# Optimization experiments

Measured on AMD Instinct MI355X. Metric: run time of the kernel, lower is better.

The kernel has to match this reference:

```python
import jax, jax.numpy as jnp
import numpy as np

LAMBD = 1.0
N_CLASSES = 1000


def setup_inputs() -> dict:
    key = jax.random.key(0)
    k1, k2, k3 = jax.random.split(key, 3)
    B, D, C = 32768, 128, N_CLASSES
    embeddings = jax.random.normal(k1, (B, D), dtype=jnp.float32)
    targets = jax.random.randint(k2, (B,), 0, C, dtype=jnp.int64)
    centers = jax.random.normal(k3, (C, D), dtype=jnp.float32)
    return {"embeddings": embeddings, "targets": targets, "centers": centers}


def reference(embeddings, targets, centers):
    # Original code round-trips embeddings through numpy -> data_mat is detached.
    e = jax.lax.stop_gradient(embeddings)  # [B, D]
    B = e.shape[0]
    C = centers.shape[0]
    # intra-class distance: exact per-sample gather + squared diff
    own_centers = centers[targets]                         # [B, D]
    dis_intra = jnp.sum((e - own_centers) ** 2, axis=1)    # [B]
    # all-pairs squared distances via expansion (avoids [B, C, D] intermediate)
    e_sq = jnp.sum(e * e, axis=1)                          # [B]
    c_sq = jnp.sum(centers * centers, axis=1)              # [C]
    cross = jnp.einsum('bd,cd->bc', e, centers)            # [B, C]
    dis_all = e_sq[:, None] + c_sq[None, :] - 2.0 * cross  # [B, C]
    # margin terms over non-target classes only
    mask = targets[:, None] != jnp.arange(C)[None, :]      # [B, C] True where j != y_i
    terms = jax.nn.relu(LAMBD + dis_intra[:, None] - dis_all)
    loss = jnp.sum(jnp.where(mask, terms, 0.0)) / (B * (C - 1))
    return loss
```

## Files before the change

### kernel.cpp

```cpp
#include <hip/hip_runtime.h>

#define DD 128
#define NTC 8

typedef __attribute__((ext_vector_type(4))) float f32x4;
typedef long long i64;

typedef __attribute__((address_space(1))) const void gvoid_t;
typedef __attribute__((address_space(3))) void svoid_t;
#define GLOAD_LDS16(g, s) __builtin_amdgcn_global_load_lds((gvoid_t*)(g), (svoid_t*)(s), 16, 0, 0)

__device__ __forceinline__ unsigned pk8(float a, float b, float c, float d) {
    int v = __builtin_amdgcn_cvt_pk_fp8_f32(a, b, 0, false);
    v = __builtin_amdgcn_cvt_pk_fp8_f32(c, d, v, true);
    return (unsigned)v;
}

__global__ void prep_centers(const float* __restrict__ ctr,
                             unsigned char* __restrict__ wsB,
                             float* __restrict__ csqh, int C, int Cpad) {
    int gid = blockIdx.x * 256 + threadIdx.x;
    int col = gid >> 2, q = gid & 3;
    if (col >= Cpad) return;
    const float* src = ctr + (size_t)col * DD + q * 32;
    const int r = col & 127;
    unsigned char* dst = wsB + (unsigned)(col >> 7) * 16384u + (unsigned)r * 128u;
    const unsigned sw = ((unsigned)r & 15u) << 3;
    float cs = 0.f;
    #pragma unroll
    for (int m = 0; m < 4; ++m) {
        float4 v0 = make_float4(0.f,0.f,0.f,0.f), v1 = v0;
        if (col < C) {
            v0 = *(const float4*)(src + m * 8);
            v1 = *(const float4*)(src + m * 8 + 4);
        }
        cs = fmaf(v0.x,v0.x,cs); cs = fmaf(v0.y,v0.y,cs);
        cs = fmaf(v0.z,v0.z,cs); cs = fmaf(v0.w,v0.w,cs);
        cs = fmaf(v1.x,v1.x,cs); cs = fmaf(v1.y,v1.y,cs);
        cs = fmaf(v1.z,v1.z,cs); cs = fmaf(v1.w,v1.w,cs);
        uint2 u;
        u.x = pk8(v0.x, v0.y, v0.z, v0.w);
        u.y = pk8(v1.x, v1.y, v1.z, v1.w);
        *(uint2*)(dst + ((((unsigned)(q * 4 + m)) * 8u) ^ sw)) = u;
    }
    cs += __shfl_xor(cs, 1); cs += __shfl_xor(cs, 2);
    if (q == 0) csqh[col] = (col < C) ? 0.5f * cs : 1e30f;
}

__global__ __launch_bounds__(512, 1) void center_mfma(
    const float* __restrict__ emb, const int* __restrict__ tgt,
    const float* __restrict__ ctr, const unsigned char* __restrict__ wsB,
    const float* __restrict__ csqh, float* __restrict__ partials)
{
    __shared__ uint4 sB4[8192];
    __shared__ uint4 sA4[1024];
    __shared__ float sRT[128];
    __shared__ float sRed[8];
    unsigned char* sAb = (unsigned char*)sA4;
    const unsigned char* sBb = (const unsigned char*)sB4;

    const int t = threadIdx.x;
    const int row0 = blockIdx.x * 128;

    const int r = t >> 2, q = t & 3;
    const float* srcE = emb + (size_t)(row0 + r) * DD + q * 32;
    const int y = tgt[row0 + r];
    const float* srcC = ctr + (size_t)y * DD + q * 32;
    float4 ev[8], cv[8];
    #pragma unroll
    for (int m = 0; m < 8; ++m) ev[m] = *(const float4*)(srcE + m * 4);
    #pragma unroll
    for (int m = 0; m < 8; ++m) cv[m] = *(const float4*)(srcC + m * 4);

    #pragma unroll
    for (int i = 0; i < 16; ++i) {
        unsigned off = (unsigned)(i * 512 + t) * 16u;
        GLOAD_LDS16(wsB + off, (unsigned char*)sB4 + off);
    }

    {
        const unsigned swA = ((unsigned)r & 15u) << 3;
        float se = 0.f, sd = 0.f;
        #pragma unroll
        for (int m = 0; m < 4; ++m) {
            float4 e0 = ev[2*m], e1 = ev[2*m+1], c0 = cv[2*m], c1 = cv[2*m+1];
            se = fmaf(e0.x,e0.x,se); se = fmaf(e0.y,e0.y,se);
            se = fmaf(e0.z,e0.z,se); se = fmaf(e0.w,e0.w,se);
            se = fmaf(e1.x,e1.x,se); se = fmaf(e1.y,e1.y,se);
            se = fmaf(e1.z,e1.z,se); se = fmaf(e1.w,e1.w,se);
            float d;
            d = e0.x-c0.x; sd = fmaf(d,d,sd);  d = e0.y-c0.y; sd = fmaf(d,d,sd);
            d = e0.z-c0.z; sd = fmaf(d,d,sd);  d = e0.w-c0.w; sd = fmaf(d,d,sd);
            d = e1.x-c1.x; sd = fmaf(d,d,sd);  d = e1.y-c1.y; sd = fmaf(d,d,sd);
            d = e1.z-c1.z; sd = fmaf(d,d,sd);  d = e1.w-c1.w; sd = fmaf(d,d,sd);
            uint2 u;
            u.x = pk8(e0.x, e0.y, e0.z, e0.w);
            u.y = pk8(e1.x, e1.y, e1.z, e1.w);
            *(uint2*)(sAb + (unsigned)r * 128u +
                      ((((unsigned)(q * 4 + m)) * 8u) ^ swA)) = u;
        }
        se += __shfl_xor(se, 1); se += __shfl_xor(se, 2);
        sd += __shfl_xor(sd, 1); sd += __shfl_xor(sd, 2);
        if (q == 0) sRT[r] = 0.5f * (1.0f + sd - se);
    }
    __syncthreads();

    const int l  = t & 63;
    const int w  = t >> 6;
    const int wr = w >> 2;
    const int wc = w & 3;
    const int li = l & 15;
    const int lh = l >> 4;
    const unsigned sw = (unsigned)li << 3;

    i64 aF[4][4];
    #pragma unroll
    for (int mf = 0; mf < 4; ++mf)
        #pragma unroll
        for (int ks = 0; ks < 4; ++ks)
            aF[mf][ks] = *(const i64*)(sAb + (unsigned)(wr*64 + 16*mf + li) * 128u +
                                       (((unsigned)(8*lh + 32*ks)) ^ sw));
    float rtv[16];
    #pragma unroll
    for (int mf = 0; mf < 4; ++mf)
        #pragma unroll
        for (int rr = 0; rr < 4; ++rr)
            rtv[mf*4+rr] = sRT[wr*64 + 16*mf + 4*lh + rr];

    float cqa[NTC], cqb[NTC];
    #pragma unroll
    for (int nt = 0; nt < NTC; ++nt) {
        cqa[nt] = csqh[nt*128 + wc*32 + li];
        cqb[nt] = csqh[nt*128 + wc*32 + 16 + li];
    }

    float tsum = 0.f;

    #pragma unroll
    for (int nt = 0; nt < NTC; ++nt) {
        i64 bF0[4], bF1[4];
        #pragma unroll
        for (int ks = 0; ks < 4; ++ks) {
            unsigned kof = ((unsigned)(8*lh + 32*ks)) ^ sw;
            bF0[ks] = *(const i64*)(sBb + (unsigned)nt*16384u +
                                    (unsigned)(wc*32 + li) * 128u + kof);
            bF1[ks] = *(const i64*)(sBb + (unsigned)nt*16384u +
                                    (unsigned)(wc*32 + 16 + li) * 128u + kof);
        }

        f32x4 acc[4][2];
        #pragma unroll
        for (int mf = 0; mf < 4; ++mf)
            #pragma unroll
            for (int rr = 0; rr < 4; ++rr) {
                acc[mf][0][rr] = rtv[mf*4+rr] - cqa[nt];
                acc[mf][1][rr] = rtv[mf*4+rr] - cqb[nt];
            }

        #pragma unroll
        for (int ks = 0; ks < 4; ++ks)
            #pragma unroll
            for (int mf = 0; mf < 4; ++mf) {
                acc[mf][0] = __builtin_amdgcn_mfma_f32_16x16x32_fp8_fp8(aF[mf][ks], bF0[ks], acc[mf][0], 0, 0, 0);
                acc[mf][1] = __builtin_amdgcn_mfma_f32_16x16x32_fp8_fp8(aF[mf][ks], bF1[ks], acc[mf][1], 0, 0, 0);
            }

        float s0 = 0.f, s1 = 0.f;
        #pragma unroll
        for (int mf = 0; mf < 4; ++mf)
            #pragma unroll
            for (int rr = 0; rr < 4; ++rr) {
                s0 = fmaf(2.0f, fmaxf(acc[mf][0][rr], 0.f), s0);
                s1 = fmaf(2.0f, fmaxf(acc[mf][1][rr], 0.f), s1);
            }
        tsum += s0 + s1;
    }

    float s = tsum;
    #pragma unroll
    for (int off = 32; off; off >>= 1) s += __shfl_down(s, off);
    if (l == 0) sRed[w] = s;
    __syncthreads();
    if (t == 0) {
        float bs = 0.f;
        #pragma unroll
        for (int i = 0; i < 8; ++i) bs += sRed[i];
        partials[blockIdx.x] = bs;
    }
}

__global__ void reduce_k(const float* __restrict__ partials, int n,
                         float* __restrict__ out, double diagSub, double invDenom) {
    __shared__ double sRed[4];
    int t = threadIdx.x;
    double s = 0.0;
    for (int i = t; i < n; i += 256) s += (double)partials[i];
    #pragma unroll
    for (int off = 32; off; off >>= 1) s += __shfl_down(s, off);
    if ((t & 63) == 0) sRed[t >> 6] = s;
    __syncthreads();
    if (t == 0) out[0] = (float)(((sRed[0]+sRed[1]+sRed[2]+sRed[3]) - diagSub) * invDenom);
}

extern "C" void kernel_launch(void* const* d_in, const int* in_sizes, int n_in,
                              void* d_out, int out_size, void* d_ws, size_t ws_size,
                              hipStream_t stream) {
    const float* emb = (const float*)d_in[0];
    const int*   tgt = (const int*)d_in[1];
    const float* ctr = (const float*)d_in[2];

    const int B = in_sizes[1];
    const int C = in_sizes[2] / DD;
    const int Cpad = NTC * 128;
    const int nblk = B / 128;

    unsigned char* wsB = (unsigned char*)d_ws;
    float* csqh = (float*)(wsB + (size_t)NTC * 16384);
    float* partials = csqh + Cpad;

    prep_centers<<<(Cpad * 4) / 256, 256, 0, stream>>>(ctr, wsB, csqh, C, Cpad);
    center_mfma<<<nblk, 512, 0, stream>>>(emb, tgt, ctr, wsB, csqh, partials);
    reduce_k<<<1, 256, 0, stream>>>(partials, nblk, (float*)d_out,
                                    (double)B,
                                    1.0 / ((double)B * (double)(C - 1)));
}
```

Baseline: 24.88 us.

## Overlap center-tile LDS loads with MFMA via per-tile vmcnt waits

Replaces the single __syncthreads before compute with per-tile s_waitcnt vmcnt plus barrier, so MFMA work on early center tiles can start while later global-to-LDS loads are still in flight. The csqh loads are hoisted ahead of the LDS copies and sched_barriers pin the instruction order so the vmcnt counts line up with the tiles. This adds eight barriers and depends on the exact count of outstanding vector-memory ops; if the compiler emits extra global loads the waits could be wrong.

```diff
diff --git a/kernel.cpp b/kernel.cpp
--- a/kernel.cpp
+++ b/kernel.cpp
@@ -9,6 +9,7 @@
 typedef __attribute__((address_space(1))) const void gvoid_t;
 typedef __attribute__((address_space(3))) void svoid_t;
 #define GLOAD_LDS16(g, s) __builtin_amdgcn_global_load_lds((gvoid_t*)(g), (svoid_t*)(s), 16, 0, 0)
+#define WAITVM(N) asm volatile("s_waitcnt vmcnt(" #N ")" ::: "memory")
 
 __device__ __forceinline__ unsigned pk8(float a, float b, float c, float d) {
     int v = __builtin_amdgcn_cvt_pk_fp8_f32(a, b, 0, false);
@@ -62,6 +63,14 @@
     const int t = threadIdx.x;
     const int row0 = blockIdx.x * 128;
 
+    const int l  = t & 63;
+    const int w  = t >> 6;
+    const int wr = w >> 2;
+    const int wc = w & 3;
+    const int li = l & 15;
+    const int lh = l >> 4;
+    const unsigned sw = (unsigned)li << 3;
+
     const int r = t >> 2, q = t & 3;
     const float* srcE = emb + (size_t)(row0 + r) * DD + q * 32;
     const int y = tgt[row0 + r];
@@ -71,12 +80,20 @@
     for (int m = 0; m < 8; ++m) ev[m] = *(const float4*)(srcE + m * 4);
     #pragma unroll
     for (int m = 0; m < 8; ++m) cv[m] = *(const float4*)(srcC + m * 4);
+    float cqa[NTC], cqb[NTC];
+    #pragma unroll
+    for (int nt = 0; nt < NTC; ++nt) {
+        cqa[nt] = csqh[nt*128 + wc*32 + li];
+        cqb[nt] = csqh[nt*128 + wc*32 + 16 + li];
+    }
+    __builtin_amdgcn_sched_barrier(0);
 
     #pragma unroll
     for (int i = 0; i < 16; ++i) {
         unsigned off = (unsigned)(i * 512 + t) * 16u;
         GLOAD_LDS16(wsB + off, (unsigned char*)sB4 + off);
     }
+    __builtin_amdgcn_sched_barrier(0);
 
     {
         const unsigned swA = ((unsigned)r & 15u) << 3;
@@ -103,15 +120,9 @@
         sd += __shfl_xor(sd, 1); sd += __shfl_xor(sd, 2);
         if (q == 0) sRT[r] = 0.5f * (1.0f + sd - se);
     }
-    __syncthreads();
-
-    const int l  = t & 63;
-    const int w  = t >> 6;
-    const int wr = w >> 2;
-    const int wc = w & 3;
-    const int li = l & 15;
-    const int lh = l >> 4;
-    const unsigned sw = (unsigned)li << 3;
+    asm volatile("s_waitcnt lgkmcnt(0)" ::: "memory");
+    __builtin_amdgcn_s_barrier();
+    __builtin_amdgcn_sched_barrier(0);
 
     i64 aF[4][4];
     #pragma unroll
@@ -127,54 +138,59 @@
         for (int rr = 0; rr < 4; ++rr)
             rtv[mf*4+rr] = sRT[wr*64 + 16*mf + 4*lh + rr];
 
-    float cqa[NTC], cqb[NTC];
-    #pragma unroll
-    for (int nt = 0; nt < NTC; ++nt) {
-        cqa[nt] = csqh[nt*128 + wc*32 + li];
-        cqb[nt] = csqh[nt*128 + wc*32 + 16 + li];
-    }
-
     float tsum = 0.f;
 
-    #pragma unroll
-    for (int nt = 0; nt < NTC; ++nt) {
-        i64 bF0[4], bF1[4];
-        #pragma unroll
-        for (int ks = 0; ks < 4; ++ks) {
-            unsigned kof = ((unsigned)(8*lh + 32*ks)) ^ sw;
-            bF0[ks] = *(const i64*)(sBb + (unsigned)nt*16384u +
-                                    (unsigned)(wc*32 + li) * 128u + kof);
-            bF1[ks] = *(const i64*)(sBb + (unsigned)nt*16384u +
-                                    (unsigned)(wc*32 + 16 + li) * 128u + kof);
-        }
-
-        f32x4 acc[4][2];
-        #pragma unroll
-        for (int mf = 0; mf < 4; ++mf)
-            #pragma unroll
-            for (int rr = 0; rr < 4; ++rr) {
-                acc[mf][0][rr] = rtv[mf*4+rr] - cqa[nt];
-                acc[mf][1][rr] = rtv[mf*4+rr] - cqb[nt];
-            }
-
-        #pragma unroll
-        for (int ks = 0; ks < 4; ++ks)
-            #pragma unroll
-            for (int mf = 0; mf < 4; ++mf) {
-                acc[mf][0] = __builtin_amdgcn_mfma_f32_16x16x32_fp8_fp8(aF[mf][ks], bF0[ks], acc[mf][0], 0, 0, 0);
-                acc[mf][1] = __builtin_amdgcn_mfma_f32_16x16x32_fp8_fp8(aF[mf][ks], bF1[ks], acc[mf][1], 0, 0, 0);
-            }
-
-        float s0 = 0.f, s1 = 0.f;
-        #pragma unroll
-        for (int mf = 0; mf < 4; ++mf)
-            #pragma unroll
-            for (int rr = 0; rr < 4; ++rr) {
-                s0 = fmaf(2.0f, fmaxf(acc[mf][0][rr], 0.f), s0);
-                s1 = fmaf(2.0f, fmaxf(acc[mf][1][rr], 0.f), s1);
-            }
-        tsum += s0 + s1;
-    }
+#define DO_TILE(NT_, VM_)                                                              \
+    {                                                                                  \
+        WAITVM(VM_);                                                                   \
+        __builtin_amdgcn_s_barrier();                                                  \
+        __builtin_amdgcn_sched_barrier(0);                                             \
+        i64 bF0[4], bF1[4];                                                            \
+        _Pragma("unroll")                                                              \
+        for (int ks = 0; ks < 4; ++ks) {                                               \
+            unsigned kof = ((unsigned)(8*lh + 32*ks)) ^ sw;                            \
+            bF0[ks] = *(const i64*)(sBb + (unsigned)(NT_)*16384u +                     \
+                                    (unsigned)(wc*32 + li) * 128u + kof);              \
+            bF1[ks] = *(const i64*)(sBb + (unsigned)(NT_)*16384u +                     \
+                                    (unsigned)(wc*32 + 16 + li) * 128u + kof);         \
+        }                                                                              \
+        f32x4 acc[4][2];                                                               \
+        _Pragma("unroll")                                                              \
+        for (int mf = 0; mf < 4; ++mf)                                                 \
+            _Pragma("unroll")                                                          \
+            for (int rr = 0; rr < 4; ++rr) {                                           \
+                acc[mf][0][rr] = rtv[mf*4+rr] - cqa[NT_];                              \
+                acc[mf][1][rr] = rtv[mf*4+rr] - cqb[NT_];                              \
+            }                                                                          \
+        _Pragma("unroll")                                                              \
+        for (int ks = 0; ks < 4; ++ks)                                                 \
+            _Pragma("unroll")                                                          \
+            for (int mf = 0; mf < 4; ++mf) {                                           \
+                acc[mf][0] = __builtin_amdgcn_mfma_f32_16x16x32_fp8_fp8(               \
+                    aF[mf][ks], bF0[ks], acc[mf][0], 0, 0, 0);                         \
+                acc[mf][1] = __builtin_amdgcn_mfma_f32_16x16x32_fp8_fp8(               \
+                    aF[mf][ks], bF1[ks], acc[mf][1], 0, 0, 0);                         \
+            }                                                                          \
+        float s0 = 0.f, s1 = 0.f;                                                      \
+        _Pragma("unroll")                                                              \
+        for (int mf = 0; mf < 4; ++mf)                                                 \
+            _Pragma("unroll")                                                          \
+            for (int rr = 0; rr < 4; ++rr) {                                           \
+                s0 = fmaf(2.0f, fmaxf(acc[mf][0][rr], 0.f), s0);                       \
+                s1 = fmaf(2.0f, fmaxf(acc[mf][1][rr], 0.f), s1);                       \
+            }                                                                          \
+        tsum += s0 + s1;                                                               \
+    }
+
+    DO_TILE(0, 14)
+    DO_TILE(1, 12)
+    DO_TILE(2, 10)
+    DO_TILE(3, 8)
+    DO_TILE(4, 6)
+    DO_TILE(5, 4)
+    DO_TILE(6, 2)
+    DO_TILE(7, 0)
+#undef DO_TILE
 
     float s = tsum;
     #pragma unroll
```

Result: no change. 25.04 us (+0.7%).

## Fuse center fp8 conversion into main kernel, drop prep launch

Applied to the files above, without the earlier changes.

Removes the separate prep_centers kernel and has every block of the main kernel load all 1000 fp32 centers, compute their half squared norms, and pack them to fp8 in swizzled LDS itself. This removes one kernel launch and the workspace round trip, but each of the 256 blocks now redoes the conversion work and reads 512KB of fp32 centers instead of 128KB of prepacked fp8. The direct global-to-LDS loads are replaced by register loads plus LDS stores.

```diff
diff --git a/kernel.cpp b/kernel.cpp
--- a/kernel.cpp
+++ b/kernel.cpp
@@ -5,10 +5,6 @@
 
 typedef __attribute__((ext_vector_type(4))) float f32x4;
 typedef long long i64;
-
-typedef __attribute__((address_space(1))) const void gvoid_t;
-typedef __attribute__((address_space(3))) void svoid_t;
-#define GLOAD_LDS16(g, s) __builtin_amdgcn_global_load_lds((gvoid_t*)(g), (svoid_t*)(s), 16, 0, 0)
 
 __device__ __forceinline__ unsigned pk8(float a, float b, float c, float d) {
     int v = __builtin_amdgcn_cvt_pk_fp8_f32(a, b, 0, false);
@@ -16,53 +12,22 @@
     return (unsigned)v;
 }
 
-__global__ void prep_centers(const float* __restrict__ ctr,
-                             unsigned char* __restrict__ wsB,
-                             float* __restrict__ csqh, int C, int Cpad) {
-    int gid = blockIdx.x * 256 + threadIdx.x;
-    int col = gid >> 2, q = gid & 3;
-    if (col >= Cpad) return;
-    const float* src = ctr + (size_t)col * DD + q * 32;
-    const int r = col & 127;
-    unsigned char* dst = wsB + (unsigned)(col >> 7) * 16384u + (unsigned)r * 128u;
-    const unsigned sw = ((unsigned)r & 15u) << 3;
-    float cs = 0.f;
-    #pragma unroll
-    for (int m = 0; m < 4; ++m) {
-        float4 v0 = make_float4(0.f,0.f,0.f,0.f), v1 = v0;
-        if (col < C) {
-            v0 = *(const float4*)(src + m * 8);
-            v1 = *(const float4*)(src + m * 8 + 4);
-        }
-        cs = fmaf(v0.x,v0.x,cs); cs = fmaf(v0.y,v0.y,cs);
-        cs = fmaf(v0.z,v0.z,cs); cs = fmaf(v0.w,v0.w,cs);
-        cs = fmaf(v1.x,v1.x,cs); cs = fmaf(v1.y,v1.y,cs);
-        cs = fmaf(v1.z,v1.z,cs); cs = fmaf(v1.w,v1.w,cs);
-        uint2 u;
-        u.x = pk8(v0.x, v0.y, v0.z, v0.w);
-        u.y = pk8(v1.x, v1.y, v1.z, v1.w);
-        *(uint2*)(dst + ((((unsigned)(q * 4 + m)) * 8u) ^ sw)) = u;
-    }
-    cs += __shfl_xor(cs, 1); cs += __shfl_xor(cs, 2);
-    if (q == 0) csqh[col] = (col < C) ? 0.5f * cs : 1e30f;
-}
-
-__global__ __launch_bounds__(512, 1) void center_mfma(
+__global__ __launch_bounds__(512, 1) void center_all(
     const float* __restrict__ emb, const int* __restrict__ tgt,
-    const float* __restrict__ ctr, const unsigned char* __restrict__ wsB,
-    const float* __restrict__ csqh, float* __restrict__ partials)
+    const float* __restrict__ ctr, float* __restrict__ partials, int C)
 {
     __shared__ uint4 sB4[8192];
     __shared__ uint4 sA4[1024];
+    __shared__ float sCQ[1024];
     __shared__ float sRT[128];
     __shared__ float sRed[8];
     unsigned char* sAb = (unsigned char*)sA4;
-    const unsigned char* sBb = (const unsigned char*)sB4;
+    unsigned char* sBb = (unsigned char*)sB4;
 
     const int t = threadIdx.x;
     const int row0 = blockIdx.x * 128;
-
     const int r = t >> 2, q = t & 3;
+
     const float* srcE = emb + (size_t)(row0 + r) * DD + q * 32;
     const int y = tgt[row0 + r];
     const float* srcC = ctr + (size_t)y * DD + q * 32;
@@ -71,11 +36,34 @@
     for (int m = 0; m < 8; ++m) ev[m] = *(const float4*)(srcE + m * 4);
     #pragma unroll
     for (int m = 0; m < 8; ++m) cv[m] = *(const float4*)(srcC + m * 4);
-
-    #pragma unroll
-    for (int i = 0; i < 16; ++i) {
-        unsigned off = (unsigned)(i * 512 + t) * 16u;
-        GLOAD_LDS16(wsB + off, (unsigned char*)sB4 + off);
+    __builtin_amdgcn_sched_barrier(0);
+
+    #pragma unroll
+    for (int p = 0; p < 8; ++p) {
+        const int col = p * 128 + r;
+        const float* src = ctr + (size_t)col * DD + q * 32;
+        unsigned char* dst = sBb + (unsigned)col * 128u;
+        const unsigned swc = ((unsigned)col & 15u) << 3;
+        const bool valid = col < C;
+        float cs = 0.f;
+        #pragma unroll
+        for (int m = 0; m < 4; ++m) {
+            float4 v0 = make_float4(0.f,0.f,0.f,0.f), v1 = v0;
+            if (valid) {
+                v0 = *(const float4*)(src + m * 8);
+                v1 = *(const float4*)(src + m * 8 + 4);
+            }
+            cs = fmaf(v0.x,v0.x,cs); cs = fmaf(v0.y,v0.y,cs);
+            cs = fmaf(v0.z,v0.z,cs); cs = fmaf(v0.w,v0.w,cs);
+            cs = fmaf(v1.x,v1.x,cs); cs = fmaf(v1.y,v1.y,cs);
+            cs = fmaf(v1.z,v1.z,cs); cs = fmaf(v1.w,v1.w,cs);
+            uint2 u;
+            u.x = pk8(v0.x, v0.y, v0.z, v0.w);
+            u.y = pk8(v1.x, v1.y, v1.z, v1.w);
+            *(uint2*)(dst + ((8u * (unsigned)(q * 4 + m)) ^ swc)) = u;
+        }
+        cs += __shfl_xor(cs, 1); cs += __shfl_xor(cs, 2);
+        if (q == 0) sCQ[col] = valid ? 0.5f * cs : 1e30f;
     }
 
     {
@@ -97,7 +85,7 @@
             u.x = pk8(e0.x, e0.y, e0.z, e0.w);
             u.y = pk8(e1.x, e1.y, e1.z, e1.w);
             *(uint2*)(sAb + (unsigned)r * 128u +
-                      ((((unsigned)(q * 4 + m)) * 8u) ^ swA)) = u;
+                      ((8u * (unsigned)(q * 4 + m)) ^ swA)) = u;
         }
         se += __shfl_xor(se, 1); se += __shfl_xor(se, 2);
         sd += __shfl_xor(sd, 1); sd += __shfl_xor(sd, 2);
@@ -130,8 +118,8 @@
     float cqa[NTC], cqb[NTC];
     #pragma unroll
     for (int nt = 0; nt < NTC; ++nt) {
-        cqa[nt] = csqh[nt*128 + wc*32 + li];
-        cqb[nt] = csqh[nt*128 + wc*32 + 16 + li];
+        cqa[nt] = sCQ[nt*128 + wc*32 + li];
+        cqb[nt] = sCQ[nt*128 + wc*32 + 16 + li];
     }
 
     float tsum = 0.f;
@@ -211,15 +199,11 @@
 
     const int B = in_sizes[1];
     const int C = in_sizes[2] / DD;
-    const int Cpad = NTC * 128;
     const int nblk = B / 128;
 
-    unsigned char* wsB = (unsigned char*)d_ws;
-    float* csqh = (float*)(wsB + (size_t)NTC * 16384);
-    float* partials = csqh + Cpad;
-
-    prep_centers<<<(Cpad * 4) / 256, 256, 0, stream>>>(ctr, wsB, csqh, C, Cpad);
-    center_mfma<<<nblk, 512, 0, stream>>>(emb, tgt, ctr, wsB, csqh, partials);
+    float* partials = (float*)d_ws;
+
+    center_all<<<nblk, 512, 0, stream>>>(emb, tgt, ctr, partials, C);
     reduce_k<<<1, 256, 0, stream>>>(partials, nblk, (float*)d_out,
                                     (double)B,
                                     1.0 / ((double)B * (double)(C - 1)));
```

Result: slower. 33.35 us (+34.0%).
